# Kernel tuning notes

Measured on AMD Instinct MI355X. Metric: run time of the kernel, lower is better.

The kernel has to match this reference:

```python
import jax, jax.numpy as jnp
import numpy as np

EPS = 1e-5

def bn_eval(x, p):
    # p: [4, C] = gamma, beta, running_mean, running_var; channel-last broadcast
    g, b, m, v = p[0], p[1], p[2], p[3]
    return (x - m) * (g / jnp.sqrt(v + EPS)) + b

def _bn_params(k, c):
    k1, k2, k3, k4 = jax.random.split(k, 4)
    gamma = jax.random.uniform(k1, (c,)) + 0.5
    beta = jax.random.normal(k2, (c,)) * 0.1
    mean = jax.random.normal(k3, (c,)) * 0.1
    var = jax.random.uniform(k4, (c,)) + 0.5
    return jnp.stack([gamma, beta, mean, var])

def _lin(k, fan_in, fan_out):
    bound = 1.0 / np.sqrt(fan_in)
    kw, kb = jax.random.split(k)
    w = jax.random.uniform(kw, (fan_in, fan_out), minval=-bound, maxval=bound)
    b = jax.random.uniform(kb, (fan_out,), minval=-bound, maxval=bound)
    return w, b

def setup_inputs() -> dict:
    key = jax.random.key(0)
    B, N, S, C, G = 2, 4096, 16, 256, 8
    ks = jax.random.split(key, 20)
    feats = jax.random.normal(ks[0], (B, N, C), dtype=jnp.float32)
    coords = jax.random.normal(ks[1], (B, N, 3), dtype=jnp.float32)
    index = jax.random.randint(ks[2], (B, N, S), 0, N, dtype=jnp.int32)
    wq, bq = _lin(ks[3], C, C); bnq = _bn_params(ks[4], C)
    wk, bk = _lin(ks[5], C, C); bnk = _bn_params(ks[6], C)
    wv, bv = _lin(ks[7], C, C)
    pm_w1, pm_b1 = _lin(ks[8], 3, C); pm_bn = _bn_params(ks[9], C)
    pm_w2, pm_b2 = _lin(ks[10], C, C)
    pb_w1, pb_b1 = _lin(ks[11], 3, C); pb_bn = _bn_params(ks[12], C)
    pb_w2, pb_b2 = _lin(ks[13], C, C)
    we_w1, we_b1 = _lin(ks[14], C, G); we_bn = _bn_params(ks[15], G)
    we_w2, we_b2 = _lin(ks[16], G, G)
    return dict(feats=feats, coords=coords, index=index,
                wq=wq, bq=bq, bnq=bnq, wk=wk, bk=bk, bnk=bnk, wv=wv, bv=bv,
                pm_w1=pm_w1, pm_b1=pm_b1, pm_bn=pm_bn, pm_w2=pm_w2, pm_b2=pm_b2,
                pb_w1=pb_w1, pb_b1=pb_b1, pb_bn=pb_bn, pb_w2=pb_w2, pb_b2=pb_b2,
                we_w1=we_w1, we_b1=we_b1, we_bn=we_bn, we_w2=we_w2, we_b2=we_b2)

def reference(feats, coords, index,
              wq, bq, bnq, wk, bk, bnk, wv, bv,
              pm_w1, pm_b1, pm_bn, pm_w2, pm_b2,
              pb_w1, pb_b1, pb_bn, pb_w2, pb_b2,
              we_w1, we_b1, we_bn, we_w2, we_b2):
    B, N, C = feats.shape
    S = index.shape[2]
    G = we_w1.shape[1]
    q = jax.nn.relu(bn_eval(feats @ wq + bq, bnq))                       # [B,N,C]
    k = jax.nn.relu(bn_eval(feats @ wk + bk, bnk))                       # [B,N,C]
    v = feats @ wv + bv                                                   # [B,N,C]
    idx = index.reshape(B, N * S)
    key_g = jnp.take_along_axis(k, idx[:, :, None], axis=1).reshape(B, N, S, C)
    val_g = jnp.take_along_axis(v, idx[:, :, None], axis=1).reshape(B, N, S, C)
    crd_g = jnp.take_along_axis(coords, idx[:, :, None], axis=1).reshape(B, N, S, 3)
    relation_qk = key_g - q[:, :, None, :]                                # [B,N,S,C]
    pos = coords[:, :, None, :] - crd_g                                   # [B,N,S,3]
    pem = jax.nn.relu(bn_eval(pos @ pm_w1 + pm_b1, pm_bn)) @ pm_w2 + pm_b2
    relation_qk = relation_qk * pem
    peb = jax.nn.relu(bn_eval(pos @ pb_w1 + pb_b1, pb_bn)) @ pb_w2 + pb_b2
    relation_qk = relation_qk + peb
    val_g = val_g + peb
    w = jax.nn.relu(bn_eval(relation_qk @ we_w1 + we_b1, we_bn)) @ we_w2 + we_b2  # [B,N,S,G]
    w = jax.nn.softmax(w, axis=2)                                         # softmax over neighbors
    val_g = val_g.reshape(B, N, S, G, C // G)
    out = jnp.einsum('bnsgi,bnsg->bngi', val_g, w).reshape(B, N, C)
    return out
```

## Files before the change

### kernel.cpp

```cpp
#include <hip/hip_runtime.h>


typedef __attribute__((ext_vector_type(8))) short bf16x8_t;
typedef __attribute__((ext_vector_type(4))) float f32x4_t;

#define BN_EPS 1e-5f

__device__ __forceinline__ float b2f(unsigned int b) {
    union { unsigned int u; float f; } x; x.u = b << 16; return x.f;
}
__device__ __forceinline__ unsigned short f2b(float f) {
    union { float f; unsigned int u; } x; x.f = f;
    return (unsigned short)((x.u + 0x7fffu + ((x.u >> 16) & 1u)) >> 16);
}
__device__ __forceinline__ unsigned int relpair(unsigned int kb, unsigned int qb,
                                                unsigned int pm_, unsigned int pb_) {
    float r0 = (b2f(kb & 0xffffu) - b2f(qb & 0xffffu)) * b2f(pm_ & 0xffffu) + b2f(pb_ & 0xffffu);
    float r1 = (b2f(kb >> 16)     - b2f(qb >> 16))     * b2f(pm_ >> 16)     + b2f(pb_ >> 16);
    return (unsigned int)f2b(r0) | ((unsigned int)f2b(r1) << 16);
}

__global__ __launch_bounds__(256) void k_prep(
    const float* __restrict__ wq, const float* __restrict__ wk,
    const float* __restrict__ wv, const float* __restrict__ pm2,
    const float* __restrict__ pb2, unsigned short* __restrict__ wsT)
{
    int mat = blockIdx.x >> 8;
    int o   = (blockIdx.x & 255) * 256 + threadIdx.x;
    const float* s = (mat == 0) ? wq : (mat == 1) ? wk : (mat == 2) ? wv
                     : (mat == 3) ? pm2 : pb2;
    int nt = o >> 12, kk = (o >> 9) & 7, lane = (o >> 3) & 63, j = o & 7;
    int k = kk * 32 + (lane >> 4) * 8 + j;
    int n = nt * 16 + (lane & 15);
    wsT[mat * 65536 + o] = f2b(s[k * 256 + n]);
}

__global__ __launch_bounds__(256) void k_qkv(
    const float* __restrict__ feats,
    const unsigned short* __restrict__ wT,
    const float* __restrict__ bq, const float* __restrict__ bnq,
    const float* __restrict__ bk, const float* __restrict__ bnk,
    const float* __restrict__ bv,
    unsigned short* __restrict__ qkv)
{
    __shared__ unsigned short A[32][264];
    const int t    = threadIdx.x;
    const int widx = blockIdx.x >> 8;
    const int mb   = blockIdx.x & 255;

    for (int i = 0; i < 8; ++i) {
        int row = 4 * i + (t >> 6), col = (t & 63) * 4;
        float4 f = *(const float4*)(feats + (mb * 32 + row) * 256 + col);
        unsigned int lo = (unsigned int)f2b(f.x) | ((unsigned int)f2b(f.y) << 16);
        unsigned int hi = (unsigned int)f2b(f.z) | ((unsigned int)f2b(f.w) << 16);
        *(uint2*)&A[row][col] = make_uint2(lo, hi);
    }
    __syncthreads();

    const int lane = t & 63, w = t >> 6;
    const int ln15 = lane & 15, quad = lane >> 4;
    const int mt = w & 1, nh = w >> 1;

    bf16x8_t afr[8];
    #pragma unroll
    for (int kk = 0; kk < 8; ++kk)
        afr[kk] = *(const bf16x8_t*)&A[mt * 16 + ln15][kk * 32 + quad * 8];

    const unsigned short* W = wT + widx * 65536;
    const float* bias = (widx == 0) ? bq : (widx == 1) ? bk : bv;
    const float* bn   = (widx == 0) ? bnq : (widx == 1) ? bnk : nullptr;
    unsigned short* dst = qkv + (size_t)widx * 8192 * 256;

    const f32x4_t fzero = {0.f, 0.f, 0.f, 0.f};
    f32x4_t acc[8];
    for (int j = 0; j < 8; ++j) acc[j] = fzero;

    #pragma unroll
    for (int kk = 0; kk < 8; ++kk) {
        #pragma unroll
        for (int j = 0; j < 8; ++j) {
            int nt = nh * 8 + j;
            bf16x8_t bfr = *(const bf16x8_t*)(W + ((nt * 8 + kk) * 64 + lane) * 8);
            acc[j] = __builtin_amdgcn_mfma_f32_16x16x32_bf16(afr[kk], bfr, acc[j], 0, 0, 0);
        }
    }

    float bb[8], sc[8], mu[8], be[8];
    #pragma unroll
    for (int j = 0; j < 8; ++j) {
        int c = (nh * 8 + j) * 16 + ln15;
        bb[j] = bias[c];
        if (bn) {
            sc[j] = bn[c] / sqrtf(bn[768 + c] + BN_EPS);
            be[j] = bn[256 + c];
            mu[j] = bn[512 + c];
        }
    }
    __syncthreads();
    #pragma unroll
    for (int j = 0; j < 8; ++j) {
        int c = (nh * 8 + j) * 16 + ln15;
        for (int r = 0; r < 4; ++r) {
            float y = acc[j][r] + bb[j];
            if (bn) y = fmaxf((y - mu[j]) * sc[j] + be[j], 0.f);
            A[mt * 16 + quad * 4 + r][c] = f2b(y);
        }
    }
    __syncthreads();
    {
        int row = t >> 3, cc = (t & 7) * 32;
        #pragma unroll
        for (int j = 0; j < 4; ++j) {
            uint4 v = *(const uint4*)&A[row][cc + 8 * j];
            *(uint4*)(dst + (mb * 32 + row) * 256 + cc + 8 * j) = v;
        }
    }
}

__global__ __launch_bounds__(256, 2) void k_main(
    const float* __restrict__ coords,
    const int*   __restrict__ index,
    const unsigned short* __restrict__ qm,
    const unsigned short* __restrict__ km,
    const unsigned short* __restrict__ vm,
    const unsigned short* __restrict__ pmw2F,
    const unsigned short* __restrict__ pbw2F,
    const float* __restrict__ pm_w1, const float* __restrict__ pm_b1,
    const float* __restrict__ pm_bn, const float* __restrict__ pm_b2,
    const float* __restrict__ pb_w1, const float* __restrict__ pb_b1,
    const float* __restrict__ pb_bn, const float* __restrict__ pb_b2,
    const float* __restrict__ we_w1, const float* __restrict__ we_b1,
    const float* __restrict__ we_bn, const float* __restrict__ we_w2,
    const float* __restrict__ we_b2,
    float* __restrict__ out)
{
    __shared__ unsigned short bufR[64][264];
    __shared__ unsigned short bufP[64][264];
    __shared__ __align__(16) char uni[8448];
    float (*Wpm)[256] = (float(*)[256])uni;
    float (*Wpb)[256] = (float(*)[256])(uni + 4096);
    unsigned short (*we1T)[264] = (unsigned short(*)[264])uni;
    float (*us_)[8] = (float(*)[8])(uni + 4224);
    float (*lg_)[8] = (float(*)[8])(uni + 6272);
    __shared__ float posA[64][4];
    __shared__ float bias2[2][256];
    __shared__ float swe[8], dwe[8], web2[8];
    __shared__ float we2s[8][8];

    const int t  = threadIdx.x;
    const int P0 = blockIdx.x * 4;
    const int b  = P0 >> 12;

    const int m3  = t >> 2;
    const int Pg3 = P0 + (m3 >> 4);
    const int rg3 = (b << 12) + index[Pg3 * 16 + (m3 & 15)];
    const int c3  = (t & 3) * 8;
    uint4 kpre[8];
    {
        const unsigned short* krow = km + rg3 * 256 + c3;
        #pragma unroll
        for (int i = 0; i < 8; ++i) kpre[i] = *(const uint4*)(krow + 32 * i);
    }
    const int p5 = t >> 6, c5 = (t & 63) * 4;
    uint2 vpre[16];
    #pragma unroll
    for (int s = 0; s < 16; ++s) {
        int rgv = (b << 12) + index[(P0 + p5) * 16 + s];
        vpre[s] = *(const uint2*)(vm + rgv * 256 + c5);
    }

    if (t < 64) {
        int p = t >> 4, s = t & 15;
        int Pg = P0 + p;
        int rg = (b << 12) + index[Pg * 16 + s];
        posA[t][0] = coords[Pg * 3 + 0] - coords[rg * 3 + 0];
        posA[t][1] = coords[Pg * 3 + 1] - coords[rg * 3 + 1];
        posA[t][2] = coords[Pg * 3 + 2] - coords[rg * 3 + 2];
        posA[t][3] = 0.f;
    }
    {
        int c = t;
        float sc = pm_bn[c] / sqrtf(pm_bn[768 + c] + BN_EPS);
        Wpm[0][c] = pm_w1[c] * sc;
        Wpm[1][c] = pm_w1[256 + c] * sc;
        Wpm[2][c] = pm_w1[512 + c] * sc;
        Wpm[3][c] = (pm_b1[c] - pm_bn[512 + c]) * sc + pm_bn[256 + c];
        sc = pb_bn[c] / sqrtf(pb_bn[768 + c] + BN_EPS);
        Wpb[0][c] = pb_w1[c] * sc;
        Wpb[1][c] = pb_w1[256 + c] * sc;
        Wpb[2][c] = pb_w1[512 + c] * sc;
        Wpb[3][c] = (pb_b1[c] - pb_bn[512 + c]) * sc + pb_bn[256 + c];
        bias2[0][c] = pb_b2[c];
        bias2[1][c] = pm_b2[c];
    }
    if (t < 8) {
        float sc = we_bn[t] / sqrtf(we_bn[24 + t] + BN_EPS);
        swe[t]  = sc;
        dwe[t]  = (we_b1[t] - we_bn[16 + t]) * sc + we_bn[8 + t];
        web2[t] = we_b2[t];
    }
    if (t < 64) we2s[t >> 3][t & 7] = we_w2[t];
    __syncthreads();

    const int lane = t & 63, w = t >> 6;
    const int ln15 = lane & 15, quad = lane >> 4;
    const int mrow = w * 16 + ln15;
    const f32x4_t fzero = {0.f, 0.f, 0.f, 0.f};

    const int hc = (t & 127) * 2;
    const int hm0 = (t >> 7) * 32;

    {
        float w00 = Wpb[0][hc], w01 = Wpb[0][hc + 1];
        float w10 = Wpb[1][hc], w11 = Wpb[1][hc + 1];
        float w20 = Wpb[2][hc], w21 = Wpb[2][hc + 1];
        float w30 = Wpb[3][hc], w31 = Wpb[3][hc + 1];
        for (int i = 0; i < 32; ++i) {
            int m = hm0 + i;
            float p0 = posA[m][0], p1 = posA[m][1], p2 = posA[m][2];
            float h0 = fmaxf(p0 * w00 + p1 * w10 + p2 * w20 + w30, 0.f);
            float h1 = fmaxf(p0 * w01 + p1 * w11 + p2 * w21 + w31, 0.f);
            *(unsigned int*)&bufR[m][hc] = (unsigned int)f2b(h0) | ((unsigned int)f2b(h1) << 16);
        }
    }
    __syncthreads();

    f32x4_t acc[4][4];
    for (int a = 0; a < 4; ++a) for (int mt = 0; mt < 4; ++mt) acc[a][mt] = fzero;
    #pragma unroll
    for (int kk = 0; kk < 8; ++kk) {
        bf16x8_t afr[4];
        #pragma unroll
        for (int mt = 0; mt < 4; ++mt)
            afr[mt] = *(const bf16x8_t*)&bufR[mt * 16 + ln15][kk * 32 + quad * 8];
        #pragma unroll
        for (int ntl = 0; ntl < 4; ++ntl) {
            int nt = w * 4 + ntl;
            bf16x8_t bfr = *(const bf16x8_t*)(pbw2F + ((nt * 8 + kk) * 64 + lane) * 8);
            #pragma unroll
            for (int mt = 0; mt < 4; ++mt)
                acc[ntl][mt] = __builtin_amdgcn_mfma_f32_16x16x32_bf16(afr[mt], bfr, acc[ntl][mt], 0, 0, 0);
        }
    }
    __syncthreads();
    #pragma unroll
    for (int ntl = 0; ntl < 4; ++ntl) {
        int c = (w * 4 + ntl) * 16 + ln15;
        float bb = bias2[0][c];
        for (int mt = 0; mt < 4; ++mt)
            for (int r = 0; r < 4; ++r)
                bufP[mt * 16 + quad * 4 + r][c] = f2b(acc[ntl][mt][r] + bb);
    }
    {
        float w00 = Wpm[0][hc], w01 = Wpm[0][hc + 1];
        float w10 = Wpm[1][hc], w11 = Wpm[1][hc + 1];
        float w20 = Wpm[2][hc], w21 = Wpm[2][hc + 1];
        float w30 = Wpm[3][hc], w31 = Wpm[3][hc + 1];
        for (int i = 0; i < 32; ++i) {
            int m = hm0 + i;
            float p0 = posA[m][0], p1 = posA[m][1], p2 = posA[m][2];
            float h0 = fmaxf(p0 * w00 + p1 * w10 + p2 * w20 + w30, 0.f);
            float h1 = fmaxf(p0 * w01 + p1 * w11 + p2 * w21 + w31, 0.f);
            *(unsigned int*)&bufR[m][hc] = (unsigned int)f2b(h0) | ((unsigned int)f2b(h1) << 16);
        }
    }
    __syncthreads();

    for (int a = 0; a < 4; ++a) for (int mt = 0; mt < 4; ++mt) acc[a][mt] = fzero;
    #pragma unroll
    for (int kk = 0; kk < 8; ++kk) {
        bf16x8_t afr[4];
        #pragma unroll
        for (int mt = 0; mt < 4; ++mt)
            afr[mt] = *(const bf16x8_t*)&bufR[mt * 16 + ln15][kk * 32 + quad * 8];
        #pragma unroll
        for (int ntl = 0; ntl < 4; ++ntl) {
            int nt = w * 4 + ntl;
            bf16x8_t bfr = *(const bf16x8_t*)(pmw2F + ((nt * 8 + kk) * 64 + lane) * 8);
            #pragma unroll
            for (int mt = 0; mt < 4; ++mt)
                acc[ntl][mt] = __builtin_amdgcn_mfma_f32_16x16x32_bf16(afr[mt], bfr, acc[ntl][mt], 0, 0, 0);
        }
    }
    __syncthreads();
    #pragma unroll
    for (int ntl = 0; ntl < 4; ++ntl) {
        int c = (w * 4 + ntl) * 16 + ln15;
        float bb = bias2[1][c];
        for (int mt = 0; mt < 4; ++mt)
            for (int r = 0; r < 4; ++r)
                bufR[mt * 16 + quad * 4 + r][c] = f2b(acc[ntl][mt][r] + bb);
    }
    __syncthreads();

    if (t < 64) {
        int g = t >> 3, j8 = t & 7;
        for (int i = 0; i < 32; ++i) {
            int c = j8 * 32 + i;
            we1T[g][c] = f2b(we_w1[c * 8 + g]);
        }
    }
    {
        const unsigned short* qrow = qm + Pg3 * 256 + c3;
        #pragma unroll
        for (int i = 0; i < 8; ++i) {
            int c = c3 + 32 * i;
            uint4 qb  = *(const uint4*)(qrow + 32 * i);
            uint4 pmv = *(const uint4*)&bufR[m3][c];
            uint4 pbv = *(const uint4*)&bufP[m3][c];
            uint4 r;
            r.x = relpair(kpre[i].x, qb.x, pmv.x, pbv.x);
            r.y = relpair(kpre[i].y, qb.y, pmv.y, pbv.y);
            r.z = relpair(kpre[i].z, qb.z, pmv.z, pbv.z);
            r.w = relpair(kpre[i].w, qb.w, pmv.w, pbv.w);
            *(uint4*)&bufR[m3][c] = r;
        }
    }
    __syncthreads();

    {
        const bf16x8_t bz = {0, 0, 0, 0, 0, 0, 0, 0};
        f32x4_t lacc = fzero;
        #pragma unroll
        for (int kk = 0; kk < 8; ++kk) {
            bf16x8_t afr = *(const bf16x8_t*)&bufR[mrow][kk * 32 + quad * 8];
            bf16x8_t bfr = bz;
            if (ln15 < 8) bfr = *(const bf16x8_t*)&we1T[ln15][kk * 32 + quad * 8];
            lacc = __builtin_amdgcn_mfma_f32_16x16x32_bf16(afr, bfr, lacc, 0, 0, 0);
        }
        if (ln15 < 8) {
            float sc = swe[ln15], dd = dwe[ln15];
            for (int r = 0; r < 4; ++r)
                us_[w * 16 + quad * 4 + r][ln15] = fmaxf(lacc[r] * sc + dd, 0.f);
        }
    }
    __syncthreads();

    if (t < 64) {
        float uv[8];
        for (int gp = 0; gp < 8; ++gp) uv[gp] = us_[t][gp];
        for (int g = 0; g < 8; ++g) {
            float l = web2[g];
            for (int gp = 0; gp < 8; ++gp) l += uv[gp] * we2s[gp][g];
            lg_[t][g] = l;
        }
    }
    __syncthreads();

    if (t < 32) {
        int p = t >> 3, g = t & 7;
        float mx = -1e30f;
        for (int s = 0; s < 16; ++s) mx = fmaxf(mx, lg_[p * 16 + s][g]);
        float e[16], sum = 0.f;
        for (int s = 0; s < 16; ++s) { e[s] = __expf(lg_[p * 16 + s][g] - mx); sum += e[s]; }
        float inv = 1.f / sum;
        for (int s = 0; s < 16; ++s) lg_[p * 16 + s][g] = e[s] * inv;
    }
    __syncthreads();

    {
        int g = c5 >> 5;
        float a0 = 0.f, a1 = 0.f, a2 = 0.f, a3 = 0.f;
        #pragma unroll
        for (int s = 0; s < 16; ++s) {
            int m = p5 * 16 + s;
            float wv_ = lg_[m][g];
            uint2 v4 = vpre[s];
            uint2 p4 = *(const uint2*)&bufP[m][c5];
            a0 += wv_ * (b2f(v4.x & 0xffffu) + b2f(p4.x & 0xffffu));
            a1 += wv_ * (b2f(v4.x >> 16)     + b2f(p4.x >> 16));
            a2 += wv_ * (b2f(v4.y & 0xffffu) + b2f(p4.y & 0xffffu));
            a3 += wv_ * (b2f(v4.y >> 16)     + b2f(p4.y >> 16));
        }
        *(float4*)(out + (size_t)(P0 + p5) * 256 + c5) = make_float4(a0, a1, a2, a3);
    }
}

extern "C" void kernel_launch(void* const* d_in, const int* in_sizes, int n_in,
                              void* d_out, int out_size, void* d_ws, size_t ws_size,
                              hipStream_t stream)
{
    const float* feats  = (const float*)d_in[0];
    const float* coords = (const float*)d_in[1];
    const int*   index  = (const int*)d_in[2];
    const float* wq     = (const float*)d_in[3];
    const float* bq     = (const float*)d_in[4];
    const float* bnq    = (const float*)d_in[5];
    const float* wk     = (const float*)d_in[6];
    const float* bk     = (const float*)d_in[7];
    const float* bnk    = (const float*)d_in[8];
    const float* wv     = (const float*)d_in[9];
    const float* bv     = (const float*)d_in[10];
    const float* pm_w1  = (const float*)d_in[11];
    const float* pm_b1  = (const float*)d_in[12];
    const float* pm_bn  = (const float*)d_in[13];
    const float* pm_w2  = (const float*)d_in[14];
    const float* pm_b2  = (const float*)d_in[15];
    const float* pb_w1  = (const float*)d_in[16];
    const float* pb_b1  = (const float*)d_in[17];
    const float* pb_bn  = (const float*)d_in[18];
    const float* pb_w2  = (const float*)d_in[19];
    const float* pb_b2  = (const float*)d_in[20];
    const float* we_w1  = (const float*)d_in[21];
    const float* we_b1  = (const float*)d_in[22];
    const float* we_bn  = (const float*)d_in[23];
    const float* we_w2  = (const float*)d_in[24];
    const float* we_b2  = (const float*)d_in[25];

    unsigned short* qkv = (unsigned short*)d_ws;
    unsigned short* wsT = qkv + (size_t)3 * 8192 * 256;

    const size_t need = ((size_t)3 * 8192 * 256 + (size_t)5 * 65536) * 2;
    if (ws_size < need) {
        hipMemsetAsync(d_out, 0, (size_t)out_size * 4, stream);
        return;
    }

    k_prep<<<5 * 256, 256, 0, stream>>>(wq, wk, wv, pm_w2, pb_w2, wsT);
    k_qkv <<<768,     256, 0, stream>>>(feats, wsT, bq, bnq, bk, bnk, bv, qkv);
    k_main<<<2048,    256, 0, stream>>>(coords, index,
                                        qkv,
                                        qkv + (size_t)8192 * 256,
                                        qkv + (size_t)2 * 8192 * 256,
                                        wsT + 3 * 65536,
                                        wsT + 4 * 65536,
                                        pm_w1, pm_b1, pm_bn, pm_b2,
                                        pb_w1, pb_b1, pb_bn, pb_b2,
                                        we_w1, we_b1, we_bn, we_w2, we_b2,
                                        (float*)d_out);
}
```

Measured before the change: 222.3 us.

## Coalesce weight prep via LDS transpose and streamline bf16 pack/unpack math

Rewrites the weight-prep kernel so each block reads a 32x64 fp32 tile with coalesced loads, transposes it through shared memory, and writes packed 16-byte MFMA fragments. The old version did strided scalar global reads and 2-byte writes across 1280 blocks. The change also adds packed bf16 conversion helpers (f2bpk, blo/bhi) that remove shifts and masks in the hot conversion paths, and reads positions with float4 loads. These are micro-optimizations across several kernels; the main kernel's structure is unchanged.

```diff
diff --git a/kernel.cpp b/kernel.cpp
--- a/kernel.cpp
+++ b/kernel.cpp
@@ -9,15 +9,30 @@
 __device__ __forceinline__ float b2f(unsigned int b) {
     union { unsigned int u; float f; } x; x.u = b << 16; return x.f;
 }
+__device__ __forceinline__ float blo(unsigned int v) {
+    union { unsigned int u; float f; } x; x.u = v << 16; return x.f;
+}
+__device__ __forceinline__ float bhi(unsigned int v) {
+    union { unsigned int u; float f; } x; x.u = v & 0xffff0000u; return x.f;
+}
+__device__ __forceinline__ unsigned int fbits(float f) {
+    union { float f; unsigned int u; } x; x.f = f; return x.u;
+}
 __device__ __forceinline__ unsigned short f2b(float f) {
-    union { float f; unsigned int u; } x; x.f = f;
-    return (unsigned short)((x.u + 0x7fffu + ((x.u >> 16) & 1u)) >> 16);
+    unsigned int u = fbits(f);
+    return (unsigned short)((u + 0x7fffu + ((u >> 16) & 1u)) >> 16);
+}
+__device__ __forceinline__ unsigned int f2bpk(float a, float b) {
+    unsigned int ua = fbits(a), ub = fbits(b);
+    unsigned int ta = ua + 0x7fffu + ((ua >> 16) & 1u);
+    unsigned int tb = ub + 0x7fffu + ((ub >> 16) & 1u);
+    return (ta >> 16) | (tb & 0xffff0000u);
 }
 __device__ __forceinline__ unsigned int relpair(unsigned int kb, unsigned int qb,
                                                 unsigned int pm_, unsigned int pb_) {
-    float r0 = (b2f(kb & 0xffffu) - b2f(qb & 0xffffu)) * b2f(pm_ & 0xffffu) + b2f(pb_ & 0xffffu);
-    float r1 = (b2f(kb >> 16)     - b2f(qb >> 16))     * b2f(pm_ >> 16)     + b2f(pb_ >> 16);
-    return (unsigned int)f2b(r0) | ((unsigned int)f2b(r1) << 16);
+    float r0 = (blo(kb) - blo(qb)) * blo(pm_) + blo(pb_);
+    float r1 = (bhi(kb) - bhi(qb)) * bhi(pm_) + bhi(pb_);
+    return f2bpk(r0, r1);
 }
 
 __global__ __launch_bounds__(256) void k_prep(
@@ -25,14 +40,36 @@
     const float* __restrict__ wv, const float* __restrict__ pm2,
     const float* __restrict__ pb2, unsigned short* __restrict__ wsT)
 {
-    int mat = blockIdx.x >> 8;
-    int o   = (blockIdx.x & 255) * 256 + threadIdx.x;
+    __shared__ unsigned short T[32][72];
+    const int bid = blockIdx.x;
+    const int mat = bid >> 5;
+    const int kk  = (bid >> 2) & 7;
+    const int ntq = bid & 3;
     const float* s = (mat == 0) ? wq : (mat == 1) ? wk : (mat == 2) ? wv
                      : (mat == 3) ? pm2 : pb2;
-    int nt = o >> 12, kk = (o >> 9) & 7, lane = (o >> 3) & 63, j = o & 7;
-    int k = kk * 32 + (lane >> 4) * 8 + j;
-    int n = nt * 16 + (lane & 15);
-    wsT[mat * 65536 + o] = f2b(s[k * 256 + n]);
+    const int t = threadIdx.x;
+    {
+        int c = t & 63, r0 = t >> 6;
+        for (int i = 0; i < 8; ++i) {
+            int r = r0 + i * 4;
+            T[r][c] = f2b(s[(kk * 32 + r) * 256 + ntq * 64 + c]);
+        }
+    }
+    __syncthreads();
+    {
+        int seg = t >> 6, lane = t & 63;
+        int col = seg * 16 + (lane & 15);
+        int kr  = (lane >> 4) * 8;
+        unsigned int v[8];
+        #pragma unroll
+        for (int j = 0; j < 8; ++j) v[j] = T[kr + j][col];
+        uint4 o;
+        o.x = v[0] | (v[1] << 16);
+        o.y = v[2] | (v[3] << 16);
+        o.z = v[4] | (v[5] << 16);
+        o.w = v[6] | (v[7] << 16);
+        *(uint4*)(wsT + mat * 65536 + (ntq * 4 + seg) * 4096 + kk * 512 + lane * 8) = o;
+    }
 }
 
 __global__ __launch_bounds__(256) void k_qkv(
@@ -51,9 +88,7 @@
     for (int i = 0; i < 8; ++i) {
         int row = 4 * i + (t >> 6), col = (t & 63) * 4;
         float4 f = *(const float4*)(feats + (mb * 32 + row) * 256 + col);
-        unsigned int lo = (unsigned int)f2b(f.x) | ((unsigned int)f2b(f.y) << 16);
-        unsigned int hi = (unsigned int)f2b(f.z) | ((unsigned int)f2b(f.w) << 16);
-        *(uint2*)&A[row][col] = make_uint2(lo, hi);
+        *(uint2*)&A[row][col] = make_uint2(f2bpk(f.x, f.y), f2bpk(f.z, f.w));
     }
     __syncthreads();
 
@@ -100,10 +135,15 @@
     #pragma unroll
     for (int j = 0; j < 8; ++j) {
         int c = (nh * 8 + j) * 16 + ln15;
+        float y[4];
         for (int r = 0; r < 4; ++r) {
-            float y = acc[j][r] + bb[j];
-            if (bn) y = fmaxf((y - mu[j]) * sc[j] + be[j], 0.f);
-            A[mt * 16 + quad * 4 + r][c] = f2b(y);
+            y[r] = acc[j][r] + bb[j];
+            if (bn) y[r] = fmaxf((y[r] - mu[j]) * sc[j] + be[j], 0.f);
+        }
+        for (int r = 0; r < 4; r += 2) {
+            unsigned int pk = f2bpk(y[r], y[r + 1]);
+            A[mt * 16 + quad * 4 + r][c]     = (unsigned short)pk;
+            A[mt * 16 + quad * 4 + r + 1][c] = (unsigned short)(pk >> 16);
         }
     }
     __syncthreads();
@@ -217,10 +257,10 @@
         float w30 = Wpb[3][hc], w31 = Wpb[3][hc + 1];
         for (int i = 0; i < 32; ++i) {
             int m = hm0 + i;
-            float p0 = posA[m][0], p1 = posA[m][1], p2 = posA[m][2];
-            float h0 = fmaxf(p0 * w00 + p1 * w10 + p2 * w20 + w30, 0.f);
-            float h1 = fmaxf(p0 * w01 + p1 * w11 + p2 * w21 + w31, 0.f);
-            *(unsigned int*)&bufR[m][hc] = (unsigned int)f2b(h0) | ((unsigned int)f2b(h1) << 16);
+            float4 p = *(const float4*)&posA[m][0];
+            float h0 = fmaxf(p.x * w00 + p.y * w10 + p.z * w20 + w30, 0.f);
+            float h1 = fmaxf(p.x * w01 + p.y * w11 + p.z * w21 + w31, 0.f);
+            *(unsigned int*)&bufR[m][hc] = f2bpk(h0, h1);
         }
     }
     __syncthreads();
@@ -248,8 +288,11 @@
         int c = (w * 4 + ntl) * 16 + ln15;
         float bb = bias2[0][c];
         for (int mt = 0; mt < 4; ++mt)
-            for (int r = 0; r < 4; ++r)
-                bufP[mt * 16 + quad * 4 + r][c] = f2b(acc[ntl][mt][r] + bb);
+            for (int r = 0; r < 4; r += 2) {
+                unsigned int pk = f2bpk(acc[ntl][mt][r] + bb, acc[ntl][mt][r + 1] + bb);
+                bufP[mt * 16 + quad * 4 + r][c]     = (unsigned short)pk;
+                bufP[mt * 16 + quad * 4 + r + 1][c] = (unsigned short)(pk >> 16);
+            }
     }
     {
         float w00 = Wpm[0][hc], w01 = Wpm[0][hc + 1];
@@ -258,10 +301,10 @@
         float w30 = Wpm[3][hc], w31 = Wpm[3][hc + 1];
         for (int i = 0; i < 32; ++i) {
             int m = hm0 + i;
-            float p0 = posA[m][0], p1 = posA[m][1], p2 = posA[m][2];
-            float h0 = fmaxf(p0 * w00 + p1 * w10 + p2 * w20 + w30, 0.f);
-            float h1 = fmaxf(p0 * w01 + p1 * w11 + p2 * w21 + w31, 0.f);
-            *(unsigned int*)&bufR[m][hc] = (unsigned int)f2b(h0) | ((unsigned int)f2b(h1) << 16);
+            float4 p = *(const float4*)&posA[m][0];
+            float h0 = fmaxf(p.x * w00 + p.y * w10 + p.z * w20 + w30, 0.f);
+            float h1 = fmaxf(p.x * w01 + p.y * w11 + p.z * w21 + w31, 0.f);
+            *(unsigned int*)&bufR[m][hc] = f2bpk(h0, h1);
         }
     }
     __syncthreads();
@@ -288,8 +331,11 @@
         int c = (w * 4 + ntl) * 16 + ln15;
         float bb = bias2[1][c];
         for (int mt = 0; mt < 4; ++mt)
-            for (int r = 0; r < 4; ++r)
-                bufR[mt * 16 + quad * 4 + r][c] = f2b(acc[ntl][mt][r] + bb);
+            for (int r = 0; r < 4; r += 2) {
+                unsigned int pk = f2bpk(acc[ntl][mt][r] + bb, acc[ntl][mt][r + 1] + bb);
+                bufR[mt * 16 + quad * 4 + r][c]     = (unsigned short)pk;
+                bufR[mt * 16 + quad * 4 + r + 1][c] = (unsigned short)(pk >> 16);
+            }
     }
     __syncthreads();
 
@@ -367,10 +413,10 @@
             float wv_ = lg_[m][g];
             uint2 v4 = vpre[s];
             uint2 p4 = *(const uint2*)&bufP[m][c5];
-            a0 += wv_ * (b2f(v4.x & 0xffffu) + b2f(p4.x & 0xffffu));
-            a1 += wv_ * (b2f(v4.x >> 16)     + b2f(p4.x >> 16));
-            a2 += wv_ * (b2f(v4.y & 0xffffu) + b2f(p4.y & 0xffffu));
-            a3 += wv_ * (b2f(v4.y >> 16)     + b2f(p4.y >> 16));
+            a0 += wv_ * (blo(v4.x) + blo(p4.x));
+            a1 += wv_ * (bhi(v4.x) + bhi(p4.x));
+            a2 += wv_ * (blo(v4.y) + blo(p4.y));
+            a3 += wv_ * (bhi(v4.y) + bhi(p4.y));
         }
         *(float4*)(out + (size_t)(P0 + p5) * 256 + c5) = make_float4(a0, a1, a2, a3);
     }
@@ -416,16 +462,16 @@
         return;
     }
 
-    k_prep<<<5 * 256, 256, 0, stream>>>(wq, wk, wv, pm_w2, pb_w2, wsT);
-    k_qkv <<<768,     256, 0, stream>>>(feats, wsT, bq, bnq, bk, bnk, bv, qkv);
-    k_main<<<2048,    256, 0, stream>>>(coords, index,
-                                        qkv,
-                                        qkv + (size_t)8192 * 256,
-                                        qkv + (size_t)2 * 8192 * 256,
-                                        wsT + 3 * 65536,
-                                        wsT + 4 * 65536,
-                                        pm_w1, pm_b1, pm_bn, pm_b2,
-                                        pb_w1, pb_b1, pb_bn, pb_b2,
-                                        we_w1, we_b1, we_bn, we_w2, we_b2,
-                                        (float*)d_out);
-}
+    k_prep<<<160,  256, 0, stream>>>(wq, wk, wv, pm_w2, pb_w2, wsT);
+    k_qkv <<<768,  256, 0, stream>>>(feats, wsT, bq, bnq, bk, bnk, bv, qkv);
+    k_main<<<2048, 256, 0, stream>>>(coords, index,
+                                     qkv,
+                                     qkv + (size_t)8192 * 256,
+                                     qkv + (size_t)2 * 8192 * 256,
+                                     wsT + 3 * 65536,
+                                     wsT + 4 * 65536,
+                                     pm_w1, pm_b1, pm_bn, pm_b2,
+                                     pb_w1, pb_b1, pb_bn, pb_b2,
+                                     we_w1, we_b1, we_bn, we_w2, we_b2,
+                                     (float*)d_out);
+}
```

Result: slower. 230.2 us (+3.6%).
